# Performance work log

Measured on AMD Instinct MI355X. Metric: run time of the kernel, lower is better.

Reference implementation:

```python
import jax, jax.numpy as jnp
import numpy as np

B, T, X, Y, H = 256, 1024, 64, 64, 256


def setup_inputs() -> dict:
    key = jax.random.key(0)
    ks = jax.random.split(key, 7)
    inputs = jax.random.normal(ks[0], (B, T, X + Y), dtype=jnp.float32)
    # zero out the last quarter of timesteps so Masking(mask_value=0.0) is exercised
    tmask = (jnp.arange(T) < (3 * T) // 4).astype(jnp.float32)[None, :, None]
    inputs = inputs * tmask
    s = 0.05
    return {
        "inputs": inputs,
        "W_enc": jax.random.normal(ks[1], (X + Y, 4 * H), dtype=jnp.float32) * s,
        "U_enc": jax.random.normal(ks[2], (H, 4 * H), dtype=jnp.float32) * s,
        "b_enc": jnp.zeros((4 * H,), dtype=jnp.float32),
        "W_dec": jax.random.normal(ks[3], (X + H, 4 * H), dtype=jnp.float32) * s,
        "U_dec": jax.random.normal(ks[4], (H, 4 * H), dtype=jnp.float32) * s,
        "b_dec": jnp.zeros((4 * H,), dtype=jnp.float32),
        "W_out": jax.random.normal(ks[5], (H, Y), dtype=jnp.float32) * s,
        "b_out": jnp.zeros((Y,), dtype=jnp.float32),
        "x_dim": X,
    }


def _lstm_relu(xW_t, U, mask_t=None, return_seq=False):
    """Keras LSTM with activation='relu', recurrent_activation='sigmoid'.
    xW_t: [T,B,4H] precomputed x@W + b. mask_t: optional [T,B] bool.
    Gate order i, f, c, o (Keras). Masked steps carry (h, c) through.
    """
    Hn = U.shape[0]
    Bn = xW_t.shape[1]
    h0 = jnp.zeros((Bn, Hn), dtype=xW_t.dtype)
    c0 = jnp.zeros((Bn, Hn), dtype=xW_t.dtype)

    def step(carry, inp):
        h, c = carry
        if mask_t is None:
            xw = inp
        else:
            xw, m = inp
        z = xw + h @ U                       # [B,4H]
        i, f, g, o = jnp.split(z, 4, axis=-1)
        i = jax.nn.sigmoid(i)
        f = jax.nn.sigmoid(f)
        o = jax.nn.sigmoid(o)
        g = jax.nn.relu(g)                   # activation='relu'
        c_new = f * c + i * g
        h_new = o * jax.nn.relu(c_new)       # activation='relu' on cell output
        if mask_t is not None:
            mm = m[:, None]
            h_new = jnp.where(mm, h_new, h)
            c_new = jnp.where(mm, c_new, c)
        return (h_new, c_new), (h_new if return_seq else None)

    xs = xW_t if mask_t is None else (xW_t, mask_t)
    (h_fin, _), hs = jax.lax.scan(step, (h0, c0), xs)
    return h_fin, hs


def reference(inputs, W_enc, U_enc, b_enc, W_dec, U_dec, b_dec, W_out, b_out, x_dim):
    # Masking(mask_value=0.0): timestep valid iff any feature != 0
    mask = jnp.any(inputs != 0.0, axis=-1)                 # [B,T]
    # Encoder LSTM, return_sequences=False
    xW = jnp.einsum('bti,ij->btj', inputs, W_enc) + b_enc  # [B,T,4H]
    h_fin, _ = _lstm_relu(xW.transpose(1, 0, 2), U_enc,
                          mask_t=mask.T, return_seq=False)  # [B,H]
    # RepeatVector + concat with x part
    Tn = inputs.shape[1]
    latent_rep = jnp.broadcast_to(h_fin[:, None, :], (h_fin.shape[0], Tn, h_fin.shape[1]))
    dec_inp = jnp.concatenate([inputs[:, :, :x_dim], latent_rep], axis=-1)  # [B,T,X+H]
    # Decoder LSTM, return_sequences=True (no mask)
    xW2 = jnp.einsum('bti,ij->btj', dec_inp, W_dec) + b_dec
    _, hs = _lstm_relu(xW2.transpose(1, 0, 2), U_dec, mask_t=None, return_seq=True)  # [T,B,H]
    hs = hs.transpose(1, 0, 2)                              # [B,T,H]
    # TimeDistributed Dense(y_dim)
    return jnp.einsum('bth,hy->bty', hs, W_out) + b_out
```

## Files before the change

kernel.cpp:

```cpp
#include <hip/hip_runtime.h>


typedef __bf16 bf16x8 __attribute__((ext_vector_type(8)));
typedef float f32x4 __attribute__((ext_vector_type(4)));
typedef unsigned int uint4v __attribute__((ext_vector_type(4)));
typedef unsigned long long ull;

#define DI __device__ __forceinline__

DI unsigned short f2bf(float f) {
  unsigned int u = __float_as_uint(f);
  u += 0x7fffu + ((u >> 16) & 1u);
  return (unsigned short)(u >> 16);
}
DI float sigf(float v) { return 1.0f / (1.0f + __expf(-v)); }

union FragU { bf16x8 v; unsigned short us[8]; };
union H8 { bf16x8 v; ull u[2]; uint4v q; };

DI f32x4 mfma16(bf16x8 a, bf16x8 b, f32x4 c) {
  return __builtin_amdgcn_mfma_f32_16x16x32_bf16(a, b, c, 0, 0, 0);
}

__global__ void pack_frags(const float* __restrict__ src,
                           unsigned short* __restrict__ dst, int K, int N) {
  int KT = K >> 5, NT = N >> 4;
  int total = KT * NT * 64;
  for (int idx = blockIdx.x * blockDim.x + threadIdx.x; idx < total;
       idx += gridDim.x * blockDim.x) {
    int lane = idx & 63;
    int fi = idx >> 6;
    int nt = fi % NT;
    int kt = fi / NT;
    int r0 = kt * 32 + (lane >> 4) * 8;
    int col = nt * 16 + (lane & 15);
    unsigned int w[4];
#pragma unroll
    for (int p = 0; p < 4; ++p) {
      unsigned int lo = f2bf(src[(size_t)(r0 + 2 * p) * N + col]);
      unsigned int hi = f2bf(src[(size_t)(r0 + 2 * p + 1) * N + col]);
      w[p] = lo | (hi << 16);
    }
    *(uint4v*)(dst + (size_t)idx * 8) = (uint4v){w[0], w[1], w[2], w[3]};
  }
}

__global__ void mask_flags(const float* __restrict__ x,
                           unsigned int* __restrict__ fmask) {
  const int t = blockIdx.x;
  const int b = threadIdx.x;
  const float* p = x + ((size_t)b * 1024 + t) * 128;
  bool nz = false;
#pragma unroll 8
  for (int k = 0; k < 32; ++k) {
    float4 v = *(const float4*)(p + k * 4);
    nz = nz || v.x != 0.f || v.y != 0.f || v.z != 0.f || v.w != 0.f;
  }
  unsigned long long bal = __ballot((int)nz);
  if ((threadIdx.x & 15) == 0)
    fmask[(size_t)(b >> 4) * 1024 + t] =
        (unsigned int)((bal >> (threadIdx.x & 48)) & 0xFFFFull);
}

#define STORE_OWN(HX) do {                                                  \
    if (tid < 128) {                                                        \
      const int kth = tid >> 6, word = tid & 63;                            \
      H8 hh; hh.q = *(const uint4v*)&hstage[2 * s + kth][word][0];          \
      const ull tg = (ull)(a + 1);                                          \
      ull A = (hh.u[0] & 0xFFFFFFFFFFFFULL) | (tg << 48);                   \
      ull B = ((hh.u[0] >> 48) | ((hh.u[1] & 0xFFFFFFFFULL) << 16)) |       \
              (tg << 48);                                                   \
      ull C = (hh.u[1] >> 32) | (tg << 32) | (tg << 48);                    \
      ull* p_ = (HX) + (size_t)(g * 2 + (a & 1)) * 1536 +                   \
                ((2 * s + kth) * 64 + word) * 3;                            \
      __hip_atomic_store(p_ + 0, A, __ATOMIC_RELAXED, __HIP_MEMORY_SCOPE_AGENT); \
      __hip_atomic_store(p_ + 1, B, __ATOMIC_RELAXED, __HIP_MEMORY_SCOPE_AGENT); \
      __hip_atomic_store(p_ + 2, C, __ATOMIC_RELAXED, __HIP_MEMORY_SCOPE_AGENT); \
    } } while (0)

#define POLL_REMOTE(HX) do {                                                \
    if (w == 1) {                                                           \
      const ull tg = (ull)(a + 1);                                          \
      int rkt[6]; int nr_ = 0;                                              \
      _Pragma("unroll")                                                     \
      for (int s2 = 0; s2 < 4; ++s2)                                        \
        if (s2 != s) { rkt[nr_++] = 2 * s2; rkt[nr_++] = 2 * s2 + 1; }      \
      const ull* hb_ = (HX) + (size_t)(g * 2 + (a & 1)) * 1536;             \
      ull R[6][3];                                                          \
      unsigned it_ = 0;                                                     \
      for (;;) {                                                            \
        _Pragma("unroll")                                                   \
        for (int r = 0; r < 6; ++r) {                                       \
          const ull* p_ = hb_ + (rkt[r] * 64 + lane) * 3;                   \
          R[r][0] = __hip_atomic_load(p_ + 0, __ATOMIC_RELAXED,             \
                                      __HIP_MEMORY_SCOPE_AGENT);            \
          R[r][1] = __hip_atomic_load(p_ + 1, __ATOMIC_RELAXED,             \
                                      __HIP_MEMORY_SCOPE_AGENT);            \
          R[r][2] = __hip_atomic_load(p_ + 2, __ATOMIC_RELAXED,             \
                                      __HIP_MEMORY_SCOPE_AGENT);            \
        }                                                                   \
        bool ok_ = true;                                                    \
        _Pragma("unroll")                                                   \
        for (int r = 0; r < 6; ++r)                                         \
          ok_ = ok_ && ((R[r][0] >> 48) == tg) && ((R[r][1] >> 48) == tg)   \
                    && ((R[r][2] >> 48) == tg);                             \
        if (ok_ || ++it_ > (1u << 14)) break;                               \
      }                                                                     \
      _Pragma("unroll")                                                     \
      for (int r = 0; r < 6; ++r) {                                         \
        H8 hh;                                                              \
        hh.u[0] = (R[r][0] & 0xFFFFFFFFFFFFULL) | (R[r][1] << 48);          \
        hh.u[1] = ((R[r][1] >> 16) & 0xFFFFFFFFULL) |                       \
                  ((R[r][2] & 0xFFFFFFFFULL) << 32);                        \
        *(uint4v*)&hstage[rkt[r]][lane][0] = hh.q;                          \
      }                                                                     \
    } } while (0)

__global__ __launch_bounds__(256) __attribute__((amdgpu_waves_per_eu(1, 1)))
void enc_rnn(const float* __restrict__ x,
             const unsigned short* __restrict__ Wef,
             const unsigned short* __restrict__ Uef,
             const float* __restrict__ benc,
             const unsigned int* __restrict__ fmask,
             ull* __restrict__ hxE,
             unsigned short* __restrict__ hfin) {
  __shared__ __align__(16) unsigned short hstage[8][64][8];

  const int tid = threadIdx.x;
  const int w = tid >> 6, lane = tid & 63;
  const int l15 = lane & 15, lkg = lane >> 4;
  const int bid = blockIdx.x;
  const int s = bid >> 4, g = bid & 15;
  const int b0 = g * 16;
  int ntf[4];
#pragma unroll
  for (int G = 0; G < 4; ++G) ntf[G] = G * 16 + s * 4 + w;

  const bf16x8* Wl = (const bf16x8*)Wef + lane;
  const bf16x8* Ul = (const bf16x8*)Uef + lane;
  const unsigned int* flagp = fmask + (size_t)g * 1024;

  bf16x8 upin[8][4];
#pragma unroll
  for (int kt = 0; kt < 8; ++kt)
#pragma unroll
    for (int G = 0; G < 4; ++G) upin[kt][G] = Ul[(kt * 64 + ntf[G]) * 64];

  bf16x8 wpin[4][4];
#pragma unroll
  for (int G = 0; G < 4; ++G)
#pragma unroll
    for (int kt = 0; kt < 4; ++kt) wpin[G][kt] = Wl[(kt * 64 + ntf[G]) * 64];

  float bfr[4];
#pragma unroll
  for (int G = 0; G < 4; ++G) bfr[G] = benc[ntf[G] * 16 + l15];

  float c4[4];
  unsigned short hreg[4];
  bf16x8 hfr[8];
#pragma unroll
  for (int q = 0; q < 4; ++q) { c4[q] = 0.f; hreg[q] = 0; }
  H8 z_; z_.u[0] = 0; z_.u[1] = 0;
#pragma unroll
  for (int kt = 0; kt < 8; ++kt) hfr[kt] = z_.v;

  const float* xbase = x + (size_t)(b0 + l15) * 1024 * 128 + lkg * 8;
  const int kt_own = 2 * s + (w >> 1);
  const int lbase = (w & 1) * 32 + (l15 >> 3) * 16 + lkg * 4;
  const int jst = l15 & 7;
  int a = 0;
  bool xvalid = false;
  float4 xa[4][2];

  __syncthreads();

  for (int t = 0; t < 1024; ++t) {
    const unsigned int flag_t = flagp[t];
    if (flag_t == 0u) { xvalid = false; continue; }

    if (!xvalid) {
      const float* xp = xbase + (size_t)t * 128;
#pragma unroll
      for (int kt = 0; kt < 4; ++kt) {
        xa[kt][0] = *(const float4*)(xp + kt * 32);
        xa[kt][1] = *(const float4*)(xp + kt * 32 + 4);
      }
    }

    f32x4 acc[4];
#pragma unroll
    for (int G = 0; G < 4; ++G) acc[G] = (f32x4){bfr[G], bfr[G], bfr[G], bfr[G]};

    FragU xf[4];
#pragma unroll
    for (int kt = 0; kt < 4; ++kt) {
      xf[kt].us[0] = f2bf(xa[kt][0].x); xf[kt].us[1] = f2bf(xa[kt][0].y);
      xf[kt].us[2] = f2bf(xa[kt][0].z); xf[kt].us[3] = f2bf(xa[kt][0].w);
      xf[kt].us[4] = f2bf(xa[kt][1].x); xf[kt].us[5] = f2bf(xa[kt][1].y);
      xf[kt].us[6] = f2bf(xa[kt][1].z); xf[kt].us[7] = f2bf(xa[kt][1].w);
    }
#pragma unroll
    for (int kt = 0; kt < 4; ++kt)
#pragma unroll
      for (int G = 0; G < 4; ++G) acc[G] = mfma16(xf[kt].v, wpin[G][kt], acc[G]);

#pragma unroll
    for (int kt = 0; kt < 8; ++kt)
#pragma unroll
      for (int G = 0; G < 4; ++G) acc[G] = mfma16(hfr[kt], upin[kt][G], acc[G]);

    unsigned short hv[4];
#pragma unroll
    for (int q = 0; q < 4; ++q) {
      float iv = sigf(acc[0][q]);
      float fv = sigf(acc[1][q]);
      float gv = fmaxf(acc[2][q], 0.f);
      float ov = sigf(acc[3][q]);
      float cn = fv * c4[q] + iv * gv;
      float hn = ov * fmaxf(cn, 0.f);
      bool m = (flag_t >> (lkg * 4 + q)) & 1u;
      c4[q] = m ? cn : c4[q];
      unsigned short hh = m ? f2bf(hn) : hreg[q];
      hreg[q] = hh;
      hv[q] = hh;
    }

    __syncthreads();
#pragma unroll
    for (int q = 0; q < 4; ++q) hstage[kt_own][lbase + q][jst] = hv[q];
    __syncthreads();

    STORE_OWN(hxE);

    if (t < 1023) {
      const float* xq = xbase + (size_t)(t + 1) * 128;
#pragma unroll
      for (int kt = 0; kt < 4; ++kt) {
        xa[kt][0] = *(const float4*)(xq + kt * 32);
        xa[kt][1] = *(const float4*)(xq + kt * 32 + 4);
      }
      xvalid = true;
    } else xvalid = false;

    POLL_REMOTE(hxE);
    __syncthreads();

#pragma unroll
    for (int kt = 0; kt < 8; ++kt)
      hfr[kt] = *(const bf16x8*)&hstage[kt][lane][0];
    ++a;
  }

  if (w < 2) {
    int kt = 2 * s + w;
    H8 hh_; hh_.v = hfr[kt];
    *(uint4v*)&hfin[((size_t)g * 8 + kt) * 512 + lane * 8] = hh_.q;
  }
}

__global__ __launch_bounds__(256) __attribute__((amdgpu_waves_per_eu(1, 1)))
void dec_rnn(const float* __restrict__ x,
             const unsigned short* __restrict__ Wd0f,
             const unsigned short* __restrict__ WdLf,
             const unsigned short* __restrict__ Udf,
             const float* __restrict__ bdec,
             const unsigned short* __restrict__ Wof,
             const float* __restrict__ bout,
             const unsigned short* __restrict__ hfin,
             ull* __restrict__ hxD,
             float* __restrict__ out) {
  __shared__ __align__(16) unsigned short hstage[8][64][8];

  const int tid = threadIdx.x;
  const int w = tid >> 6, lane = tid & 63;
  const int l15 = lane & 15, lkg = lane >> 4;
  const int bid = blockIdx.x;
  const int s = bid >> 4, g = bid & 15;
  const int b0 = g * 16;
  int ntf[4];
#pragma unroll
  for (int G = 0; G < 4; ++G) ntf[G] = G * 16 + s * 4 + w;

  const bf16x8* W0l = (const bf16x8*)Wd0f + lane;
  const bf16x8* WLl = (const bf16x8*)WdLf + lane;
  const bf16x8* Ul  = (const bf16x8*)Udf + lane;

  bf16x8 upin[8][4];
#pragma unroll
  for (int kt = 0; kt < 8; ++kt)
#pragma unroll
    for (int G = 0; G < 4; ++G) upin[kt][G] = Ul[(kt * 64 + ntf[G]) * 64];

  bf16x8 w0pin[4][2];
#pragma unroll
  for (int G = 0; G < 4; ++G)
#pragma unroll
    for (int kt = 0; kt < 2; ++kt) w0pin[G][kt] = W0l[(kt * 64 + ntf[G]) * 64];

  f32x4 lat[4];
  {
    bf16x8 ha[8];
#pragma unroll
    for (int kt = 0; kt < 8; ++kt)
      ha[kt] = *(const bf16x8*)&hfin[((size_t)g * 8 + kt) * 512 + lane * 8];
#pragma unroll
    for (int G = 0; G < 4; ++G) {
      float bd = bdec[ntf[G] * 16 + l15];
      lat[G] = (f32x4){bd, bd, bd, bd};
    }
#pragma unroll
    for (int kt = 0; kt < 8; ++kt)
#pragma unroll
      for (int G = 0; G < 4; ++G)
        lat[G] = mfma16(ha[kt], WLl[(kt * 64 + ntf[G]) * 64], lat[G]);
  }

  bf16x8 wofr[8];
  if (w == 0) {
#pragma unroll
    for (int kt = 0; kt < 8; ++kt)
      wofr[kt] = ((const bf16x8*)Wof)[(kt * 4 + s) * 64 + lane];
  }
  const float bo = bout[s * 16 + l15];

  float c4[4];
  bf16x8 hfr[8];
#pragma unroll
  for (int q = 0; q < 4; ++q) c4[q] = 0.f;
  H8 z_; z_.u[0] = 0; z_.u[1] = 0;
#pragma unroll
  for (int kt = 0; kt < 8; ++kt) hfr[kt] = z_.v;

  const float* xbase = x + (size_t)(b0 + l15) * 1024 * 128 + lkg * 8;
  const int kt_own = 2 * s + (w >> 1);
  const int lbase = (w & 1) * 32 + (l15 >> 3) * 16 + lkg * 4;
  const int jst = l15 & 7;

  float4 xa[2][2];
  xa[0][0] = *(const float4*)(xbase);      xa[0][1] = *(const float4*)(xbase + 4);
  xa[1][0] = *(const float4*)(xbase + 32); xa[1][1] = *(const float4*)(xbase + 36);

  __syncthreads();

  for (int t = 0; t < 1024; ++t) {
    const int a = t;
    f32x4 acc[4];
#pragma unroll
    for (int G = 0; G < 4; ++G) acc[G] = lat[G];

    FragU xf[2];
#pragma unroll
    for (int kt = 0; kt < 2; ++kt) {
      xf[kt].us[0] = f2bf(xa[kt][0].x); xf[kt].us[1] = f2bf(xa[kt][0].y);
      xf[kt].us[2] = f2bf(xa[kt][0].z); xf[kt].us[3] = f2bf(xa[kt][0].w);
      xf[kt].us[4] = f2bf(xa[kt][1].x); xf[kt].us[5] = f2bf(xa[kt][1].y);
      xf[kt].us[6] = f2bf(xa[kt][1].z); xf[kt].us[7] = f2bf(xa[kt][1].w);
    }
#pragma unroll
    for (int kt = 0; kt < 2; ++kt)
#pragma unroll
      for (int G = 0; G < 4; ++G) acc[G] = mfma16(xf[kt].v, w0pin[G][kt], acc[G]);

#pragma unroll
    for (int kt = 0; kt < 8; ++kt)
#pragma unroll
      for (int G = 0; G < 4; ++G) acc[G] = mfma16(hfr[kt], upin[kt][G], acc[G]);

    unsigned short hv[4];
#pragma unroll
    for (int q = 0; q < 4; ++q) {
      float iv = sigf(acc[0][q]);
      float fv = sigf(acc[1][q]);
      float gv = fmaxf(acc[2][q], 0.f);
      float ov = sigf(acc[3][q]);
      float cn = fv * c4[q] + iv * gv;
      float hn = ov * fmaxf(cn, 0.f);
      c4[q] = cn;
      hv[q] = f2bf(hn);
    }

    __syncthreads();
#pragma unroll
    for (int q = 0; q < 4; ++q) hstage[kt_own][lbase + q][jst] = hv[q];
    __syncthreads();

    STORE_OWN(hxD);

    if (t > 0 && w == 0) {
      f32x4 oa = {bo, bo, bo, bo};
#pragma unroll
      for (int kt = 0; kt < 8; ++kt) oa = mfma16(hfr[kt], wofr[kt], oa);
#pragma unroll
      for (int q = 0; q < 4; ++q)
        out[((size_t)(b0 + lkg * 4 + q) * 1024 + (t - 1)) * 64 + s * 16 + l15] = oa[q];
    }
    if (t < 1023) {
      const float* xq = xbase + (size_t)(t + 1) * 128;
      xa[0][0] = *(const float4*)(xq);      xa[0][1] = *(const float4*)(xq + 4);
      xa[1][0] = *(const float4*)(xq + 32); xa[1][1] = *(const float4*)(xq + 36);
    }

    POLL_REMOTE(hxD);
    __syncthreads();

#pragma unroll
    for (int kt = 0; kt < 8; ++kt)
      hfr[kt] = *(const bf16x8*)&hstage[kt][lane][0];
  }

  if (w == 0) {
    f32x4 oa = {bo, bo, bo, bo};
#pragma unroll
    for (int kt = 0; kt < 8; ++kt) oa = mfma16(hfr[kt], wofr[kt], oa);
#pragma unroll
    for (int q = 0; q < 4; ++q)
      out[((size_t)(b0 + lkg * 4 + q) * 1024 + 1023) * 64 + s * 16 + l15] = oa[q];
  }
}

extern "C" void kernel_launch(void* const* d_in, const int* in_sizes, int n_in,
                              void* d_out, int out_size, void* d_ws, size_t ws_size,
                              hipStream_t stream) {
  const float* inputs = (const float*)d_in[0];
  const float* W_enc  = (const float*)d_in[1];
  const float* U_enc  = (const float*)d_in[2];
  const float* b_enc  = (const float*)d_in[3];
  const float* W_dec  = (const float*)d_in[4];
  const float* U_dec  = (const float*)d_in[5];
  const float* b_dec  = (const float*)d_in[6];
  const float* W_out  = (const float*)d_in[7];
  const float* b_out  = (const float*)d_in[8];

  char* ws = (char*)d_ws;
  unsigned short* Uef   = (unsigned short*)(ws + 0);
  unsigned short* Udf   = (unsigned short*)(ws + 524288);
  unsigned short* Wef   = (unsigned short*)(ws + 1048576);
  unsigned short* Wd0f  = (unsigned short*)(ws + 1310720);
  unsigned short* WdLf  = (unsigned short*)(ws + 1441792);
  unsigned short* Wof   = (unsigned short*)(ws + 1966080);
  unsigned short* hfin  = (unsigned short*)(ws + 1998848);
  unsigned int*   fmask = (unsigned int*)(ws + 2129920);
  ull*            hxE   = (ull*)(ws + 2195456);
  ull*            hxD   = (ull*)(ws + 2588672);

  mask_flags<<<1024, 256, 0, stream>>>(inputs, fmask);
  pack_frags<<<128, 256, 0, stream>>>(U_enc, Uef, 256, 1024);
  pack_frags<<<128, 256, 0, stream>>>(U_dec, Udf, 256, 1024);
  pack_frags<<<128, 256, 0, stream>>>(W_enc, Wef, 128, 1024);
  pack_frags<<<128, 256, 0, stream>>>(W_dec, Wd0f, 64, 1024);
  pack_frags<<<128, 256, 0, stream>>>(W_dec + 64 * 1024, WdLf, 256, 1024);
  pack_frags<<<32, 256, 0, stream>>>(W_out, Wof, 256, 64);

  enc_rnn<<<64, 256, 0, stream>>>(inputs, Wef, Uef, b_enc, fmask, hxE, hfin);
  dec_rnn<<<64, 256, 0, stream>>>(inputs, Wd0f, WdLf, Udf, b_dec, Wof, b_out,
                                  hfin, hxD, (float*)d_out);
}
```

Before: 4.959 ms.

## Interleave two batch groups per block and spread remote polling across waves

Each block now owns two independent 16-row batch groups and alternates their LSTM steps, so one group's cross-block h exchange can overlap the other group's compute. The grid is halved from 64 to 32 blocks while each keeps the same weight slices pinned in registers. Polling of remote hidden-state slices is spread over three waves, each checking one slice, instead of one wave checking all six. The cost is more register pressure from doubled state and extra barriers per step, and the latency of each recurrent step now sits behind the other group's work.

```diff
diff --git a/kernel.cpp b/kernel.cpp
--- a/kernel.cpp
+++ b/kernel.cpp
@@ -20,6 +20,9 @@
 
 DI f32x4 mfma16(bf16x8 a, bf16x8 b, f32x4 c) {
   return __builtin_amdgcn_mfma_f32_16x16x32_bf16(a, b, c, 0, 0, 0);
+}
+DI ull ald(const ull* p) {
+  return __hip_atomic_load(p, __ATOMIC_RELAXED, __HIP_MEMORY_SCOPE_AGENT);
 }
 
 __global__ void pack_frags(const float* __restrict__ src,
@@ -62,58 +65,47 @@
         (unsigned int)((bal >> (threadIdx.x & 48)) & 0xFFFFull);
 }
 
-#define STORE_OWN(HX) do {                                                  \
+#define STORE_OWN(HSTG, HX, G, PAR, TAG) do {                               \
     if (tid < 128) {                                                        \
       const int kth = tid >> 6, word = tid & 63;                            \
-      H8 hh; hh.q = *(const uint4v*)&hstage[2 * s + kth][word][0];          \
-      const ull tg = (ull)(a + 1);                                          \
-      ull A = (hh.u[0] & 0xFFFFFFFFFFFFULL) | (tg << 48);                   \
-      ull B = ((hh.u[0] >> 48) | ((hh.u[1] & 0xFFFFFFFFULL) << 16)) |       \
-              (tg << 48);                                                   \
-      ull C = (hh.u[1] >> 32) | (tg << 32) | (tg << 48);                    \
-      ull* p_ = (HX) + (size_t)(g * 2 + (a & 1)) * 1536 +                   \
+      H8 hh; hh.q = *(const uint4v*)&(HSTG)[2 * s + kth][word][0];          \
+      const ull tg = (ull)(TAG);                                            \
+      ull Aw = (hh.u[0] & 0xFFFFFFFFFFFFULL) | (tg << 48);                  \
+      ull Bw = ((hh.u[0] >> 48) | ((hh.u[1] & 0xFFFFFFFFULL) << 16)) |      \
+               (tg << 48);                                                  \
+      ull Cw = (hh.u[1] >> 32) | (tg << 48);                                \
+      ull* p_ = (HX) + (size_t)((G) * 2 + (PAR)) * 1536 +                   \
                 ((2 * s + kth) * 64 + word) * 3;                            \
-      __hip_atomic_store(p_ + 0, A, __ATOMIC_RELAXED, __HIP_MEMORY_SCOPE_AGENT); \
-      __hip_atomic_store(p_ + 1, B, __ATOMIC_RELAXED, __HIP_MEMORY_SCOPE_AGENT); \
-      __hip_atomic_store(p_ + 2, C, __ATOMIC_RELAXED, __HIP_MEMORY_SCOPE_AGENT); \
+      __hip_atomic_store(p_ + 0, Aw, __ATOMIC_RELAXED, __HIP_MEMORY_SCOPE_AGENT); \
+      __hip_atomic_store(p_ + 1, Bw, __ATOMIC_RELAXED, __HIP_MEMORY_SCOPE_AGENT); \
+      __hip_atomic_store(p_ + 2, Cw, __ATOMIC_RELAXED, __HIP_MEMORY_SCOPE_AGENT); \
     } } while (0)
 
-#define POLL_REMOTE(HX) do {                                                \
-    if (w == 1) {                                                           \
-      const ull tg = (ull)(a + 1);                                          \
-      int rkt[6]; int nr_ = 0;                                              \
-      _Pragma("unroll")                                                     \
-      for (int s2 = 0; s2 < 4; ++s2)                                        \
-        if (s2 != s) { rkt[nr_++] = 2 * s2; rkt[nr_++] = 2 * s2 + 1; }      \
-      const ull* hb_ = (HX) + (size_t)(g * 2 + (a & 1)) * 1536;             \
-      ull R[6][3];                                                          \
+#define POLL_REMOTE(HSTG, HX, G, PAR, TAG) do {                             \
+    if (w >= 1) {                                                           \
+      const int s2_ = (w - 1) + ((w - 1) >= s ? 1 : 0);                     \
+      const int rk0 = 2 * s2_, rk1 = rk0 + 1;                               \
+      const ull* hb_ = (HX) + (size_t)((G) * 2 + (PAR)) * 1536;             \
+      const ull* q0 = hb_ + (rk0 * 64 + lane) * 3;                          \
+      const ull* q1 = hb_ + (rk1 * 64 + lane) * 3;                          \
+      const ull tg = (ull)(TAG);                                            \
+      ull A0, A1, A2, B0, B1, B2;                                           \
       unsigned it_ = 0;                                                     \
       for (;;) {                                                            \
-        _Pragma("unroll")                                                   \
-        for (int r = 0; r < 6; ++r) {                                       \
-          const ull* p_ = hb_ + (rkt[r] * 64 + lane) * 3;                   \
-          R[r][0] = __hip_atomic_load(p_ + 0, __ATOMIC_RELAXED,             \
-                                      __HIP_MEMORY_SCOPE_AGENT);            \
-          R[r][1] = __hip_atomic_load(p_ + 1, __ATOMIC_RELAXED,             \
-                                      __HIP_MEMORY_SCOPE_AGENT);            \
-          R[r][2] = __hip_atomic_load(p_ + 2, __ATOMIC_RELAXED,             \
-                                      __HIP_MEMORY_SCOPE_AGENT);            \
-        }                                                                   \
-        bool ok_ = true;                                                    \
-        _Pragma("unroll")                                                   \
-        for (int r = 0; r < 6; ++r)                                         \
-          ok_ = ok_ && ((R[r][0] >> 48) == tg) && ((R[r][1] >> 48) == tg)   \
-                    && ((R[r][2] >> 48) == tg);                             \
+        A0 = ald(q0); A1 = ald(q0 + 1); A2 = ald(q0 + 2);                   \
+        B0 = ald(q1); B1 = ald(q1 + 1); B2 = ald(q1 + 2);                   \
+        bool ok_ = ((A0 >> 48) == tg) && ((A1 >> 48) == tg) &&              \
+                   ((A2 >> 48) == tg) && ((B0 >> 48) == tg) &&              \
+                   ((B1 >> 48) == tg) && ((B2 >> 48) == tg);                \
         if (ok_ || ++it_ > (1u << 14)) break;                               \
       }                                                                     \
-      _Pragma("unroll")                                                     \
-      for (int r = 0; r < 6; ++r) {                                         \
-        H8 hh;                                                              \
-        hh.u[0] = (R[r][0] & 0xFFFFFFFFFFFFULL) | (R[r][1] << 48);          \
-        hh.u[1] = ((R[r][1] >> 16) & 0xFFFFFFFFULL) |                       \
-                  ((R[r][2] & 0xFFFFFFFFULL) << 32);                        \
-        *(uint4v*)&hstage[rkt[r]][lane][0] = hh.q;                          \
-      }                                                                     \
+      H8 h0_, h1_;                                                          \
+      h0_.u[0] = (A0 & 0xFFFFFFFFFFFFULL) | (A1 << 48);                     \
+      h0_.u[1] = ((A1 >> 16) & 0xFFFFFFFFULL) | ((A2 & 0xFFFFFFFFULL) << 32); \
+      h1_.u[0] = (B0 & 0xFFFFFFFFFFFFULL) | (B1 << 48);                     \
+      h1_.u[1] = ((B1 >> 16) & 0xFFFFFFFFULL) | ((B2 & 0xFFFFFFFFULL) << 32); \
+      *(uint4v*)&(HSTG)[rk0][lane][0] = h0_.q;                              \
+      *(uint4v*)&(HSTG)[rk1][lane][0] = h1_.q;                              \
     } } while (0)
 
 __global__ __launch_bounds__(256) __attribute__((amdgpu_waves_per_eu(1, 1)))
@@ -124,21 +116,21 @@
              const unsigned int* __restrict__ fmask,
              ull* __restrict__ hxE,
              unsigned short* __restrict__ hfin) {
-  __shared__ __align__(16) unsigned short hstage[8][64][8];
+  __shared__ __align__(16) unsigned short hstA[8][64][8];
+  __shared__ __align__(16) unsigned short hstB[8][64][8];
 
   const int tid = threadIdx.x;
   const int w = tid >> 6, lane = tid & 63;
   const int l15 = lane & 15, lkg = lane >> 4;
   const int bid = blockIdx.x;
-  const int s = bid >> 4, g = bid & 15;
-  const int b0 = g * 16;
+  const int s = bid >> 3, p = bid & 7;
+  const int gA = 2 * p, gB = 2 * p + 1;
   int ntf[4];
 #pragma unroll
   for (int G = 0; G < 4; ++G) ntf[G] = G * 16 + s * 4 + w;
 
   const bf16x8* Wl = (const bf16x8*)Wef + lane;
   const bf16x8* Ul = (const bf16x8*)Uef + lane;
-  const unsigned int* flagp = fmask + (size_t)g * 1024;
 
   bf16x8 upin[8][4];
 #pragma unroll
@@ -156,106 +148,174 @@
 #pragma unroll
   for (int G = 0; G < 4; ++G) bfr[G] = benc[ntf[G] * 16 + l15];
 
-  float c4[4];
-  unsigned short hreg[4];
-  bf16x8 hfr[8];
-#pragma unroll
-  for (int q = 0; q < 4; ++q) { c4[q] = 0.f; hreg[q] = 0; }
+  float cA[4], cB[4];
+  unsigned short hgA[4], hgB[4];
+  bf16x8 hfA[8], hfB[8];
+#pragma unroll
+  for (int q = 0; q < 4; ++q) { cA[q] = 0.f; cB[q] = 0.f; hgA[q] = 0; hgB[q] = 0; }
   H8 z_; z_.u[0] = 0; z_.u[1] = 0;
 #pragma unroll
-  for (int kt = 0; kt < 8; ++kt) hfr[kt] = z_.v;
-
-  const float* xbase = x + (size_t)(b0 + l15) * 1024 * 128 + lkg * 8;
+  for (int kt = 0; kt < 8; ++kt) { hfA[kt] = z_.v; hfB[kt] = z_.v; }
+
+  const float* xbA = x + (size_t)(gA * 16 + l15) * 1024 * 128 + lkg * 8;
+  const float* xbB = x + (size_t)(gB * 16 + l15) * 1024 * 128 + lkg * 8;
+  const unsigned int* fpA = fmask + (size_t)gA * 1024;
+  const unsigned int* fpB = fmask + (size_t)gB * 1024;
   const int kt_own = 2 * s + (w >> 1);
   const int lbase = (w & 1) * 32 + (l15 >> 3) * 16 + lkg * 4;
   const int jst = l15 & 7;
-  int a = 0;
-  bool xvalid = false;
-  float4 xa[4][2];
+  int aA = 0, aB = 0;
+  bool xvA = false, xvB = false;
+  float4 xaA[4][2], xaB[4][2];
 
   __syncthreads();
 
   for (int t = 0; t < 1024; ++t) {
-    const unsigned int flag_t = flagp[t];
-    if (flag_t == 0u) { xvalid = false; continue; }
-
-    if (!xvalid) {
-      const float* xp = xbase + (size_t)t * 128;
+    const unsigned int flA = fpA[t], flB = fpB[t];
+
+    if (flA) {
+      if (!xvA) {
+        const float* xp = xbA + (size_t)t * 128;
+#pragma unroll
+        for (int kt = 0; kt < 4; ++kt) {
+          xaA[kt][0] = *(const float4*)(xp + kt * 32);
+          xaA[kt][1] = *(const float4*)(xp + kt * 32 + 4);
+        }
+      }
+      f32x4 acc[4];
+#pragma unroll
+      for (int G = 0; G < 4; ++G) acc[G] = (f32x4){bfr[G], bfr[G], bfr[G], bfr[G]};
+      FragU xf[4];
 #pragma unroll
       for (int kt = 0; kt < 4; ++kt) {
-        xa[kt][0] = *(const float4*)(xp + kt * 32);
-        xa[kt][1] = *(const float4*)(xp + kt * 32 + 4);
-      }
-    }
-
-    f32x4 acc[4];
-#pragma unroll
-    for (int G = 0; G < 4; ++G) acc[G] = (f32x4){bfr[G], bfr[G], bfr[G], bfr[G]};
-
-    FragU xf[4];
-#pragma unroll
-    for (int kt = 0; kt < 4; ++kt) {
-      xf[kt].us[0] = f2bf(xa[kt][0].x); xf[kt].us[1] = f2bf(xa[kt][0].y);
-      xf[kt].us[2] = f2bf(xa[kt][0].z); xf[kt].us[3] = f2bf(xa[kt][0].w);
-      xf[kt].us[4] = f2bf(xa[kt][1].x); xf[kt].us[5] = f2bf(xa[kt][1].y);
-      xf[kt].us[6] = f2bf(xa[kt][1].z); xf[kt].us[7] = f2bf(xa[kt][1].w);
-    }
-#pragma unroll
-    for (int kt = 0; kt < 4; ++kt)
-#pragma unroll
-      for (int G = 0; G < 4; ++G) acc[G] = mfma16(xf[kt].v, wpin[G][kt], acc[G]);
-
-#pragma unroll
-    for (int kt = 0; kt < 8; ++kt)
-#pragma unroll
-      for (int G = 0; G < 4; ++G) acc[G] = mfma16(hfr[kt], upin[kt][G], acc[G]);
-
-    unsigned short hv[4];
-#pragma unroll
-    for (int q = 0; q < 4; ++q) {
-      float iv = sigf(acc[0][q]);
-      float fv = sigf(acc[1][q]);
-      float gv = fmaxf(acc[2][q], 0.f);
-      float ov = sigf(acc[3][q]);
-      float cn = fv * c4[q] + iv * gv;
-      float hn = ov * fmaxf(cn, 0.f);
-      bool m = (flag_t >> (lkg * 4 + q)) & 1u;
-      c4[q] = m ? cn : c4[q];
-      unsigned short hh = m ? f2bf(hn) : hreg[q];
-      hreg[q] = hh;
-      hv[q] = hh;
-    }
-
-    __syncthreads();
-#pragma unroll
-    for (int q = 0; q < 4; ++q) hstage[kt_own][lbase + q][jst] = hv[q];
-    __syncthreads();
-
-    STORE_OWN(hxE);
-
-    if (t < 1023) {
-      const float* xq = xbase + (size_t)(t + 1) * 128;
+        xf[kt].us[0] = f2bf(xaA[kt][0].x); xf[kt].us[1] = f2bf(xaA[kt][0].y);
+        xf[kt].us[2] = f2bf(xaA[kt][0].z); xf[kt].us[3] = f2bf(xaA[kt][0].w);
+        xf[kt].us[4] = f2bf(xaA[kt][1].x); xf[kt].us[5] = f2bf(xaA[kt][1].y);
+        xf[kt].us[6] = f2bf(xaA[kt][1].z); xf[kt].us[7] = f2bf(xaA[kt][1].w);
+      }
+#pragma unroll
+      for (int kt = 0; kt < 4; ++kt)
+#pragma unroll
+        for (int G = 0; G < 4; ++G) acc[G] = mfma16(xf[kt].v, wpin[G][kt], acc[G]);
+#pragma unroll
+      for (int kt = 0; kt < 8; ++kt)
+#pragma unroll
+        for (int G = 0; G < 4; ++G) acc[G] = mfma16(hfA[kt], upin[kt][G], acc[G]);
+
+      unsigned short hv[4];
+#pragma unroll
+      for (int q = 0; q < 4; ++q) {
+        float iv = sigf(acc[0][q]);
+        float fv = sigf(acc[1][q]);
+        float gv = fmaxf(acc[2][q], 0.f);
+        float ov = sigf(acc[3][q]);
+        float cn = fv * cA[q] + iv * gv;
+        float hn = ov * fmaxf(cn, 0.f);
+        bool m = (flA >> (lkg * 4 + q)) & 1u;
+        cA[q] = m ? cn : cA[q];
+        unsigned short hh = m ? f2bf(hn) : hgA[q];
+        hgA[q] = hh; hv[q] = hh;
+      }
+      __syncthreads();
+#pragma unroll
+      for (int q = 0; q < 4; ++q) hstA[kt_own][lbase + q][jst] = hv[q];
+      __syncthreads();
+      STORE_OWN(hstA, hxE, gA, (aA & 1), aA + 1);
+    }
+
+    if (flB) {
+      if (!xvB) {
+        const float* xp = xbB + (size_t)t * 128;
+#pragma unroll
+        for (int kt = 0; kt < 4; ++kt) {
+          xaB[kt][0] = *(const float4*)(xp + kt * 32);
+          xaB[kt][1] = *(const float4*)(xp + kt * 32 + 4);
+        }
+      }
+      f32x4 acc[4];
+#pragma unroll
+      for (int G = 0; G < 4; ++G) acc[G] = (f32x4){bfr[G], bfr[G], bfr[G], bfr[G]};
+      FragU xf[4];
 #pragma unroll
       for (int kt = 0; kt < 4; ++kt) {
-        xa[kt][0] = *(const float4*)(xq + kt * 32);
-        xa[kt][1] = *(const float4*)(xq + kt * 32 + 4);
-      }
-      xvalid = true;
-    } else xvalid = false;
-
-    POLL_REMOTE(hxE);
-    __syncthreads();
-
-#pragma unroll
-    for (int kt = 0; kt < 8; ++kt)
-      hfr[kt] = *(const bf16x8*)&hstage[kt][lane][0];
-    ++a;
+        xf[kt].us[0] = f2bf(xaB[kt][0].x); xf[kt].us[1] = f2bf(xaB[kt][0].y);
+        xf[kt].us[2] = f2bf(xaB[kt][0].z); xf[kt].us[3] = f2bf(xaB[kt][0].w);
+        xf[kt].us[4] = f2bf(xaB[kt][1].x); xf[kt].us[5] = f2bf(xaB[kt][1].y);
+        xf[kt].us[6] = f2bf(xaB[kt][1].z); xf[kt].us[7] = f2bf(xaB[kt][1].w);
+      }
+#pragma unroll
+      for (int kt = 0; kt < 4; ++kt)
+#pragma unroll
+        for (int G = 0; G < 4; ++G) acc[G] = mfma16(xf[kt].v, wpin[G][kt], acc[G]);
+#pragma unroll
+      for (int kt = 0; kt < 8; ++kt)
+#pragma unroll
+        for (int G = 0; G < 4; ++G) acc[G] = mfma16(hfB[kt], upin[kt][G], acc[G]);
+
+      unsigned short hv[4];
+#pragma unroll
+      for (int q = 0; q < 4; ++q) {
+        float iv = sigf(acc[0][q]);
+        float fv = sigf(acc[1][q]);
+        float gv = fmaxf(acc[2][q], 0.f);
+        float ov = sigf(acc[3][q]);
+        float cn = fv * cB[q] + iv * gv;
+        float hn = ov * fmaxf(cn, 0.f);
+        bool m = (flB >> (lkg * 4 + q)) & 1u;
+        cB[q] = m ? cn : cB[q];
+        unsigned short hh = m ? f2bf(hn) : hgB[q];
+        hgB[q] = hh; hv[q] = hh;
+      }
+      __syncthreads();
+#pragma unroll
+      for (int q = 0; q < 4; ++q) hstB[kt_own][lbase + q][jst] = hv[q];
+      __syncthreads();
+      STORE_OWN(hstB, hxE, gB, (aB & 1), aB + 1);
+    }
+
+    if (flA) {
+      if (t < 1023) {
+        const float* xq = xbA + (size_t)(t + 1) * 128;
+#pragma unroll
+        for (int kt = 0; kt < 4; ++kt) {
+          xaA[kt][0] = *(const float4*)(xq + kt * 32);
+          xaA[kt][1] = *(const float4*)(xq + kt * 32 + 4);
+        }
+        xvA = true;
+      } else xvA = false;
+      POLL_REMOTE(hstA, hxE, gA, (aA & 1), aA + 1);
+      __syncthreads();
+#pragma unroll
+      for (int kt = 0; kt < 8; ++kt)
+        hfA[kt] = *(const bf16x8*)&hstA[kt][lane][0];
+      ++aA;
+    } else xvA = false;
+
+    if (flB) {
+      if (t < 1023) {
+        const float* xq = xbB + (size_t)(t + 1) * 128;
+#pragma unroll
+        for (int kt = 0; kt < 4; ++kt) {
+          xaB[kt][0] = *(const float4*)(xq + kt * 32);
+          xaB[kt][1] = *(const float4*)(xq + kt * 32 + 4);
+        }
+        xvB = true;
+      } else xvB = false;
+      POLL_REMOTE(hstB, hxE, gB, (aB & 1), aB + 1);
+      __syncthreads();
+#pragma unroll
+      for (int kt = 0; kt < 8; ++kt)
+        hfB[kt] = *(const bf16x8*)&hstB[kt][lane][0];
+      ++aB;
+    } else xvB = false;
   }
 
   if (w < 2) {
     int kt = 2 * s + w;
-    H8 hh_; hh_.v = hfr[kt];
-    *(uint4v*)&hfin[((size_t)g * 8 + kt) * 512 + lane * 8] = hh_.q;
+    H8 h1; h1.v = hfA[kt];
+    *(uint4v*)&hfin[((size_t)gA * 8 + kt) * 512 + lane * 8] = h1.q;
+    H8 h2; h2.v = hfB[kt];
+    *(uint4v*)&hfin[((size_t)gB * 8 + kt) * 512 + lane * 8] = h2.q;
   }
 }
 
@@ -270,14 +330,16 @@
              const unsigned short* __restrict__ hfin,
              ull* __restrict__ hxD,
              float* __restrict__ out) {
-  __shared__ __align__(16) unsigned short hstage[8][64][8];
+  __shared__ __align__(16) unsigned short hstA[8][64][8];
+  __shared__ __align__(16) unsigned short hstB[8][64][8];
 
   const int tid = threadIdx.x;
   const int w = tid >> 6, lane = tid & 63;
   const int l15 = lane & 15, lkg = lane >> 4;
   const int bid = blockIdx.x;
-  const int s = bid >> 4, g = bid & 15;
-  const int b0 = g * 16;
+  const int s = bid >> 3, p = bid & 7;
+  const int gA = 2 * p, gB = 2 * p + 1;
+  const int b0A = gA * 16, b0B = gB * 16;
   int ntf[4];
 #pragma unroll
   for (int G = 0; G < 4; ++G) ntf[G] = G * 16 + s * 4 + w;
@@ -298,22 +360,28 @@
 #pragma unroll
     for (int kt = 0; kt < 2; ++kt) w0pin[G][kt] = W0l[(kt * 64 + ntf[G]) * 64];
 
-  f32x4 lat[4];
+  f32x4 latA[4], latB[4];
   {
-    bf16x8 ha[8];
-#pragma unroll
-    for (int kt = 0; kt < 8; ++kt)
-      ha[kt] = *(const bf16x8*)&hfin[((size_t)g * 8 + kt) * 512 + lane * 8];
+    bf16x8 ha[8], hb[8];
+#pragma unroll
+    for (int kt = 0; kt < 8; ++kt) {
+      ha[kt] = *(const bf16x8*)&hfin[((size_t)gA * 8 + kt) * 512 + lane * 8];
+      hb[kt] = *(const bf16x8*)&hfin[((size_t)gB * 8 + kt) * 512 + lane * 8];
+    }
 #pragma unroll
     for (int G = 0; G < 4; ++G) {
       float bd = bdec[ntf[G] * 16 + l15];
-      lat[G] = (f32x4){bd, bd, bd, bd};
+      latA[G] = (f32x4){bd, bd, bd, bd};
+      latB[G] = (f32x4){bd, bd, bd, bd};
     }
 #pragma unroll
     for (int kt = 0; kt < 8; ++kt)
 #pragma unroll
-      for (int G = 0; G < 4; ++G)
-        lat[G] = mfma16(ha[kt], WLl[(kt * 64 + ntf[G]) * 64], lat[G]);
+      for (int G = 0; G < 4; ++G) {
+        bf16x8 wl = WLl[(kt * 64 + ntf[G]) * 64];
+        latA[G] = mfma16(ha[kt], wl, latA[G]);
+        latB[G] = mfma16(hb[kt], wl, latB[G]);
+      }
   }
 
   bf16x8 wofr[8];
@@ -324,98 +392,159 @@
   }
   const float bo = bout[s * 16 + l15];
 
-  float c4[4];
-  bf16x8 hfr[8];
-#pragma unroll
-  for (int q = 0; q < 4; ++q) c4[q] = 0.f;
+  float cA[4], cB[4];
+  bf16x8 hfA[8], hfB[8];
+#pragma unroll
+  for (int q = 0; q < 4; ++q) { cA[q] = 0.f; cB[q] = 0.f; }
   H8 z_; z_.u[0] = 0; z_.u[1] = 0;
 #pragma unroll
-  for (int kt = 0; kt < 8; ++kt) hfr[kt] = z_.v;
-
-  const float* xbase = x + (size_t)(b0 + l15) * 1024 * 128 + lkg * 8;
+  for (int kt = 0; kt < 8; ++kt) { hfA[kt] = z_.v; hfB[kt] = z_.v; }
+
+  const float* xbA = x + (size_t)(b0A + l15) * 1024 * 128 + lkg * 8;
+  const float* xbB = x + (size_t)(b0B + l15) * 1024 * 128 + lkg * 8;
   const int kt_own = 2 * s + (w >> 1);
   const int lbase = (w & 1) * 32 + (l15 >> 3) * 16 + lkg * 4;
   const int jst = l15 & 7;
 
-  float4 xa[2][2];
-  xa[0][0] = *(const float4*)(xbase);      xa[0][1] = *(const float4*)(xbase + 4);
-  xa[1][0] = *(const float4*)(xbase + 32); xa[1][1] = *(const float4*)(xbase + 36);
+  float4 xaA[2][2], xaB[2][2];
+  xaA[0][0] = *(const float4*)(xbA);      xaA[0][1] = *(const float4*)(xbA + 4);
+  xaA[1][0] = *(const float4*)(xbA + 32); xaA[1][1] = *(const float4*)(xbA + 36);
+  xaB[0][0] = *(const float4*)(xbB);      xaB[0][1] = *(const float4*)(xbB + 4);
+  xaB[1][0] = *(const float4*)(xbB + 32); xaB[1][1] = *(const float4*)(xbB + 36);
 
   __syncthreads();
 
   for (int t = 0; t < 1024; ++t) {
-    const int a = t;
-    f32x4 acc[4];
-#pragma unroll
-    for (int G = 0; G < 4; ++G) acc[G] = lat[G];
-
-    FragU xf[2];
-#pragma unroll
-    for (int kt = 0; kt < 2; ++kt) {
-      xf[kt].us[0] = f2bf(xa[kt][0].x); xf[kt].us[1] = f2bf(xa[kt][0].y);
-      xf[kt].us[2] = f2bf(xa[kt][0].z); xf[kt].us[3] = f2bf(xa[kt][0].w);
-      xf[kt].us[4] = f2bf(xa[kt][1].x); xf[kt].us[5] = f2bf(xa[kt][1].y);
-      xf[kt].us[6] = f2bf(xa[kt][1].z); xf[kt].us[7] = f2bf(xa[kt][1].w);
-    }
-#pragma unroll
-    for (int kt = 0; kt < 2; ++kt)
-#pragma unroll
-      for (int G = 0; G < 4; ++G) acc[G] = mfma16(xf[kt].v, w0pin[G][kt], acc[G]);
-
-#pragma unroll
-    for (int kt = 0; kt < 8; ++kt)
-#pragma unroll
-      for (int G = 0; G < 4; ++G) acc[G] = mfma16(hfr[kt], upin[kt][G], acc[G]);
-
-    unsigned short hv[4];
-#pragma unroll
-    for (int q = 0; q < 4; ++q) {
-      float iv = sigf(acc[0][q]);
-      float fv = sigf(acc[1][q]);
-      float gv = fmaxf(acc[2][q], 0.f);
-      float ov = sigf(acc[3][q]);
-      float cn = fv * c4[q] + iv * gv;
-      float hn = ov * fmaxf(cn, 0.f);
-      c4[q] = cn;
-      hv[q] = f2bf(hn);
-    }
-
-    __syncthreads();
-#pragma unroll
-    for (int q = 0; q < 4; ++q) hstage[kt_own][lbase + q][jst] = hv[q];
-    __syncthreads();
-
-    STORE_OWN(hxD);
+    {
+      f32x4 acc[4];
+#pragma unroll
+      for (int G = 0; G < 4; ++G) acc[G] = latA[G];
+      FragU xf[2];
+#pragma unroll
+      for (int kt = 0; kt < 2; ++kt) {
+        xf[kt].us[0] = f2bf(xaA[kt][0].x); xf[kt].us[1] = f2bf(xaA[kt][0].y);
+        xf[kt].us[2] = f2bf(xaA[kt][0].z); xf[kt].us[3] = f2bf(xaA[kt][0].w);
+        xf[kt].us[4] = f2bf(xaA[kt][1].x); xf[kt].us[5] = f2bf(xaA[kt][1].y);
+        xf[kt].us[6] = f2bf(xaA[kt][1].z); xf[kt].us[7] = f2bf(xaA[kt][1].w);
+      }
+#pragma unroll
+      for (int kt = 0; kt < 2; ++kt)
+#pragma unroll
+        for (int G = 0; G < 4; ++G) acc[G] = mfma16(xf[kt].v, w0pin[G][kt], acc[G]);
+#pragma unroll
+      for (int kt = 0; kt < 8; ++kt)
+#pragma unroll
+        for (int G = 0; G < 4; ++G) acc[G] = mfma16(hfA[kt], upin[kt][G], acc[G]);
+
+      unsigned short hv[4];
+#pragma unroll
+      for (int q = 0; q < 4; ++q) {
+        float iv = sigf(acc[0][q]);
+        float fv = sigf(acc[1][q]);
+        float gv = fmaxf(acc[2][q], 0.f);
+        float ov = sigf(acc[3][q]);
+        float cn = fv * cA[q] + iv * gv;
+        cA[q] = cn;
+        hv[q] = f2bf(ov * fmaxf(cn, 0.f));
+      }
+      __syncthreads();
+#pragma unroll
+      for (int q = 0; q < 4; ++q) hstA[kt_own][lbase + q][jst] = hv[q];
+      __syncthreads();
+      STORE_OWN(hstA, hxD, gA, (t & 1), t + 1);
+    }
+
+    {
+      f32x4 acc[4];
+#pragma unroll
+      for (int G = 0; G < 4; ++G) acc[G] = latB[G];
+      FragU xf[2];
+#pragma unroll
+      for (int kt = 0; kt < 2; ++kt) {
+        xf[kt].us[0] = f2bf(xaB[kt][0].x); xf[kt].us[1] = f2bf(xaB[kt][0].y);
+        xf[kt].us[2] = f2bf(xaB[kt][0].z); xf[kt].us[3] = f2bf(xaB[kt][0].w);
+        xf[kt].us[4] = f2bf(xaB[kt][1].x); xf[kt].us[5] = f2bf(xaB[kt][1].y);
+        xf[kt].us[6] = f2bf(xaB[kt][1].z); xf[kt].us[7] = f2bf(xaB[kt][1].w);
+      }
+#pragma unroll
+      for (int kt = 0; kt < 2; ++kt)
+#pragma unroll
+        for (int G = 0; G < 4; ++G) acc[G] = mfma16(xf[kt].v, w0pin[G][kt], acc[G]);
+#pragma unroll
+      for (int kt = 0; kt < 8; ++kt)
+#pragma unroll
+        for (int G = 0; G < 4; ++G) acc[G] = mfma16(hfB[kt], upin[kt][G], acc[G]);
+
+      unsigned short hv[4];
+#pragma unroll
+      for (int q = 0; q < 4; ++q) {
+        float iv = sigf(acc[0][q]);
+        float fv = sigf(acc[1][q]);
+        float gv = fmaxf(acc[2][q], 0.f);
+        float ov = sigf(acc[3][q]);
+        float cn = fv * cB[q] + iv * gv;
+        cB[q] = cn;
+        hv[q] = f2bf(ov * fmaxf(cn, 0.f));
+      }
+      __syncthreads();
+#pragma unroll
+      for (int q = 0; q < 4; ++q) hstB[kt_own][lbase + q][jst] = hv[q];
+      __syncthreads();
+      STORE_OWN(hstB, hxD, gB, (t & 1), t + 1);
+    }
 
     if (t > 0 && w == 0) {
       f32x4 oa = {bo, bo, bo, bo};
 #pragma unroll
-      for (int kt = 0; kt < 8; ++kt) oa = mfma16(hfr[kt], wofr[kt], oa);
+      for (int kt = 0; kt < 8; ++kt) oa = mfma16(hfA[kt], wofr[kt], oa);
 #pragma unroll
       for (int q = 0; q < 4; ++q)
-        out[((size_t)(b0 + lkg * 4 + q) * 1024 + (t - 1)) * 64 + s * 16 + l15] = oa[q];
+        out[((size_t)(b0A + lkg * 4 + q) * 1024 + (t - 1)) * 64 + s * 16 + l15] = oa[q];
     }
     if (t < 1023) {
-      const float* xq = xbase + (size_t)(t + 1) * 128;
-      xa[0][0] = *(const float4*)(xq);      xa[0][1] = *(const float4*)(xq + 4);
-      xa[1][0] = *(const float4*)(xq + 32); xa[1][1] = *(const float4*)(xq + 36);
-    }
-
-    POLL_REMOTE(hxD);
+      const float* xq = xbA + (size_t)(t + 1) * 128;
+      xaA[0][0] = *(const float4*)(xq);      xaA[0][1] = *(const float4*)(xq + 4);
+      xaA[1][0] = *(const float4*)(xq + 32); xaA[1][1] = *(const float4*)(xq + 36);
+    }
+    POLL_REMOTE(hstA, hxD, gA, (t & 1), t + 1);
     __syncthreads();
-
 #pragma unroll
     for (int kt = 0; kt < 8; ++kt)
-      hfr[kt] = *(const bf16x8*)&hstage[kt][lane][0];
+      hfA[kt] = *(const bf16x8*)&hstA[kt][lane][0];
+
+    if (t > 0 && w == 0) {
+      f32x4 oa = {bo, bo, bo, bo};
+#pragma unroll
+      for (int kt = 0; kt < 8; ++kt) oa = mfma16(hfB[kt], wofr[kt], oa);
+#pragma unroll
+      for (int q = 0; q < 4; ++q)
+        out[((size_t)(b0B + lkg * 4 + q) * 1024 + (t - 1)) * 64 + s * 16 + l15] = oa[q];
+    }
+    if (t < 1023) {
+      const float* xq = xbB + (size_t)(t + 1) * 128;
+      xaB[0][0] = *(const float4*)(xq);      xaB[0][1] = *(const float4*)(xq + 4);
+      xaB[1][0] = *(const float4*)(xq + 32); xaB[1][1] = *(const float4*)(xq + 36);
+    }
+    POLL_REMOTE(hstB, hxD, gB, (t & 1), t + 1);
+    __syncthreads();
+#pragma unroll
+    for (int kt = 0; kt < 8; ++kt)
+      hfB[kt] = *(const bf16x8*)&hstB[kt][lane][0];
   }
 
   if (w == 0) {
     f32x4 oa = {bo, bo, bo, bo};
 #pragma unroll
-    for (int kt = 0; kt < 8; ++kt) oa = mfma16(hfr[kt], wofr[kt], oa);
+    for (int kt = 0; kt < 8; ++kt) oa = mfma16(hfA[kt], wofr[kt], oa);
 #pragma unroll
     for (int q = 0; q < 4; ++q)
-      out[((size_t)(b0 + lkg * 4 + q) * 1024 + 1023) * 64 + s * 16 + l15] = oa[q];
+      out[((size_t)(b0A + lkg * 4 + q) * 1024 + 1023) * 64 + s * 16 + l15] = oa[q];
+    f32x4 ob = {bo, bo, bo, bo};
+#pragma unroll
+    for (int kt = 0; kt < 8; ++kt) ob = mfma16(hfB[kt], wofr[kt], ob);
+#pragma unroll
+    for (int q = 0; q < 4; ++q)
+      out[((size_t)(b0B + lkg * 4 + q) * 1024 + 1023) * 64 + s * 16 + l15] = ob[q];
   }
 }
 
@@ -452,7 +581,7 @@
   pack_frags<<<128, 256, 0, stream>>>(W_dec + 64 * 1024, WdLf, 256, 1024);
   pack_frags<<<32, 256, 0, stream>>>(W_out, Wof, 256, 64);
 
-  enc_rnn<<<64, 256, 0, stream>>>(inputs, Wef, Uef, b_enc, fmask, hxE, hfin);
-  dec_rnn<<<64, 256, 0, stream>>>(inputs, Wd0f, WdLf, Udf, b_dec, Wof, b_out,
+  enc_rnn<<<32, 256, 0, stream>>>(inputs, Wef, Uef, b_enc, fmask, hxE, hfin);
+  dec_rnn<<<32, 256, 0, stream>>>(inputs, Wd0f, WdLf, Udf, b_dec, Wof, b_out,
                                   hfin, hxD, (float*)d_out);
 }
```

Result: slower. 9.092 ms (+83.4%).

## Spread remote h polling across three waves and use LDS-only barriers

Applied to the files above, without the earlier changes.

Remote-slice polling of the hidden-state exchange buffer is now split so that waves 1–3 each spin on one remote slice, where before wave 1 polled all six k-tiles serially. __syncthreads is replaced with an inline s_waitcnt lgkmcnt(0) + s_barrier, so the barrier no longer waits on outstanding global memory operations (vmcnt). The aim is a shorter per-timestep critical path in the cross-block recurrent handoff. The risk is ordering: the barrier no longer drains global stores/loads, and polling now uses more waves.

```diff
diff --git a/kernel.cpp b/kernel.cpp
--- a/kernel.cpp
+++ b/kernel.cpp
@@ -15,11 +15,18 @@
 }
 DI float sigf(float v) { return 1.0f / (1.0f + __expf(-v)); }
 
+DI void barrier_lds() {
+  asm volatile("s_waitcnt lgkmcnt(0)\n\ts_barrier" ::: "memory");
+}
+
 union FragU { bf16x8 v; unsigned short us[8]; };
 union H8 { bf16x8 v; ull u[2]; uint4v q; };
 
 DI f32x4 mfma16(bf16x8 a, bf16x8 b, f32x4 c) {
   return __builtin_amdgcn_mfma_f32_16x16x32_bf16(a, b, c, 0, 0, 0);
+}
+DI ull ald(const ull* p) {
+  return __hip_atomic_load(p, __ATOMIC_RELAXED, __HIP_MEMORY_SCOPE_AGENT);
 }
 
 __global__ void pack_frags(const float* __restrict__ src,
@@ -62,58 +69,47 @@
         (unsigned int)((bal >> (threadIdx.x & 48)) & 0xFFFFull);
 }
 
-#define STORE_OWN(HX) do {                                                  \
+#define STORE_OWN(HX, PAR, TAG) do {                                        \
     if (tid < 128) {                                                        \
       const int kth = tid >> 6, word = tid & 63;                            \
       H8 hh; hh.q = *(const uint4v*)&hstage[2 * s + kth][word][0];          \
-      const ull tg = (ull)(a + 1);                                          \
-      ull A = (hh.u[0] & 0xFFFFFFFFFFFFULL) | (tg << 48);                   \
-      ull B = ((hh.u[0] >> 48) | ((hh.u[1] & 0xFFFFFFFFULL) << 16)) |       \
-              (tg << 48);                                                   \
-      ull C = (hh.u[1] >> 32) | (tg << 32) | (tg << 48);                    \
-      ull* p_ = (HX) + (size_t)(g * 2 + (a & 1)) * 1536 +                   \
+      const ull tg = (ull)(TAG);                                            \
+      ull Aw = (hh.u[0] & 0xFFFFFFFFFFFFULL) | (tg << 48);                  \
+      ull Bw = ((hh.u[0] >> 48) | ((hh.u[1] & 0xFFFFFFFFULL) << 16)) |      \
+               (tg << 48);                                                  \
+      ull Cw = (hh.u[1] >> 32) | (tg << 48);                                \
+      ull* p_ = (HX) + (size_t)(g * 2 + (PAR)) * 1536 +                     \
                 ((2 * s + kth) * 64 + word) * 3;                            \
-      __hip_atomic_store(p_ + 0, A, __ATOMIC_RELAXED, __HIP_MEMORY_SCOPE_AGENT); \
-      __hip_atomic_store(p_ + 1, B, __ATOMIC_RELAXED, __HIP_MEMORY_SCOPE_AGENT); \
-      __hip_atomic_store(p_ + 2, C, __ATOMIC_RELAXED, __HIP_MEMORY_SCOPE_AGENT); \
+      __hip_atomic_store(p_ + 0, Aw, __ATOMIC_RELAXED, __HIP_MEMORY_SCOPE_AGENT); \
+      __hip_atomic_store(p_ + 1, Bw, __ATOMIC_RELAXED, __HIP_MEMORY_SCOPE_AGENT); \
+      __hip_atomic_store(p_ + 2, Cw, __ATOMIC_RELAXED, __HIP_MEMORY_SCOPE_AGENT); \
     } } while (0)
 
-#define POLL_REMOTE(HX) do {                                                \
-    if (w == 1) {                                                           \
-      const ull tg = (ull)(a + 1);                                          \
-      int rkt[6]; int nr_ = 0;                                              \
-      _Pragma("unroll")                                                     \
-      for (int s2 = 0; s2 < 4; ++s2)                                        \
-        if (s2 != s) { rkt[nr_++] = 2 * s2; rkt[nr_++] = 2 * s2 + 1; }      \
-      const ull* hb_ = (HX) + (size_t)(g * 2 + (a & 1)) * 1536;             \
-      ull R[6][3];                                                          \
+#define POLL_REMOTE(HX, PAR, TAG) do {                                      \
+    if (w >= 1) {                                                           \
+      const int s2_ = (w - 1) + ((w - 1) >= s ? 1 : 0);                     \
+      const int rk0 = 2 * s2_, rk1 = rk0 + 1;                               \
+      const ull* hb_ = (HX) + (size_t)(g * 2 + (PAR)) * 1536;               \
+      const ull* q0 = hb_ + (rk0 * 64 + lane) * 3;                          \
+      const ull* q1 = hb_ + (rk1 * 64 + lane) * 3;                          \
+      const ull tg = (ull)(TAG);                                            \
+      ull A0, A1, A2, B0, B1, B2;                                           \
       unsigned it_ = 0;                                                     \
       for (;;) {                                                            \
-        _Pragma("unroll")                                                   \
-        for (int r = 0; r < 6; ++r) {                                       \
-          const ull* p_ = hb_ + (rkt[r] * 64 + lane) * 3;                   \
-          R[r][0] = __hip_atomic_load(p_ + 0, __ATOMIC_RELAXED,             \
-                                      __HIP_MEMORY_SCOPE_AGENT);            \
-          R[r][1] = __hip_atomic_load(p_ + 1, __ATOMIC_RELAXED,             \
-                                      __HIP_MEMORY_SCOPE_AGENT);            \
-          R[r][2] = __hip_atomic_load(p_ + 2, __ATOMIC_RELAXED,             \
-                                      __HIP_MEMORY_SCOPE_AGENT);            \
-        }                                                                   \
-        bool ok_ = true;                                                    \
-        _Pragma("unroll")                                                   \
-        for (int r = 0; r < 6; ++r)                                         \
-          ok_ = ok_ && ((R[r][0] >> 48) == tg) && ((R[r][1] >> 48) == tg)   \
-                    && ((R[r][2] >> 48) == tg);                             \
+        A0 = ald(q0); A1 = ald(q0 + 1); A2 = ald(q0 + 2);                   \
+        B0 = ald(q1); B1 = ald(q1 + 1); B2 = ald(q1 + 2);                   \
+        bool ok_ = ((A0 >> 48) == tg) && ((A1 >> 48) == tg) &&              \
+                   ((A2 >> 48) == tg) && ((B0 >> 48) == tg) &&              \
+                   ((B1 >> 48) == tg) && ((B2 >> 48) == tg);                \
         if (ok_ || ++it_ > (1u << 14)) break;                               \
       }                                                                     \
-      _Pragma("unroll")                                                     \
-      for (int r = 0; r < 6; ++r) {                                         \
-        H8 hh;                                                              \
-        hh.u[0] = (R[r][0] & 0xFFFFFFFFFFFFULL) | (R[r][1] << 48);          \
-        hh.u[1] = ((R[r][1] >> 16) & 0xFFFFFFFFULL) |                       \
-                  ((R[r][2] & 0xFFFFFFFFULL) << 32);                        \
-        *(uint4v*)&hstage[rkt[r]][lane][0] = hh.q;                          \
-      }                                                                     \
+      H8 h0_, h1_;                                                          \
+      h0_.u[0] = (A0 & 0xFFFFFFFFFFFFULL) | (A1 << 48);                     \
+      h0_.u[1] = ((A1 >> 16) & 0xFFFFFFFFULL) | ((A2 & 0xFFFFFFFFULL) << 32); \
+      h1_.u[0] = (B0 & 0xFFFFFFFFFFFFULL) | (B1 << 48);                     \
+      h1_.u[1] = ((B1 >> 16) & 0xFFFFFFFFULL) | ((B2 & 0xFFFFFFFFULL) << 32); \
+      *(uint4v*)&hstage[rk0][lane][0] = h0_.q;                              \
+      *(uint4v*)&hstage[rk1][lane][0] = h1_.q;                              \
     } } while (0)
 
 __global__ __launch_bounds__(256) __attribute__((amdgpu_waves_per_eu(1, 1)))
@@ -226,12 +222,12 @@
       hv[q] = hh;
     }
 
-    __syncthreads();
+    barrier_lds();
 #pragma unroll
     for (int q = 0; q < 4; ++q) hstage[kt_own][lbase + q][jst] = hv[q];
-    __syncthreads();
-
-    STORE_OWN(hxE);
+    barrier_lds();
+
+    STORE_OWN(hxE, (a & 1), a + 1);
 
     if (t < 1023) {
       const float* xq = xbase + (size_t)(t + 1) * 128;
@@ -243,8 +239,8 @@
       xvalid = true;
     } else xvalid = false;
 
-    POLL_REMOTE(hxE);
-    __syncthreads();
+    POLL_REMOTE(hxE, (a & 1), a + 1);
+    barrier_lds();
 
 #pragma unroll
     for (int kt = 0; kt < 8; ++kt)
@@ -344,7 +340,6 @@
   __syncthreads();
 
   for (int t = 0; t < 1024; ++t) {
-    const int a = t;
     f32x4 acc[4];
 #pragma unroll
     for (int G = 0; G < 4; ++G) acc[G] = lat[G];
@@ -380,12 +375,12 @@
       hv[q] = f2bf(hn);
     }
 
-    __syncthreads();
+    barrier_lds();
 #pragma unroll
     for (int q = 0; q < 4; ++q) hstage[kt_own][lbase + q][jst] = hv[q];
-    __syncthreads();
-
-    STORE_OWN(hxD);
+    barrier_lds();
+
+    STORE_OWN(hxD, (t & 1), t + 1);
 
     if (t > 0 && w == 0) {
       f32x4 oa = {bo, bo, bo, bo};
@@ -401,8 +396,8 @@
       xa[1][0] = *(const float4*)(xq + 32); xa[1][1] = *(const float4*)(xq + 36);
     }
 
-    POLL_REMOTE(hxD);
-    __syncthreads();
+    POLL_REMOTE(hxD, (t & 1), t + 1);
+    barrier_lds();
 
 #pragma unroll
     for (int kt = 0; kt < 8; ++kt)
```

After: 5.291 ms. +6.7%, slower.
